# Kernel optimization log

Hardware: AMD Instinct MI355X
Metric: run time of the kernel (lower is better)

Reference implementation:

```python
import jax, jax.numpy as jnp
import numpy as np

B, J, D = 64, 512, 1024

def setup_inputs() -> dict:
    key = jax.random.key(0)
    k_x, k_m, k1, k2, k3 = jax.random.split(key, 5)
    x = jax.random.normal(k_x, (B, J, D), dtype=jnp.float32)
    mask = (jax.random.uniform(k_m, (B, J)) > 0.1).astype(jnp.float32)
    s1 = 1.0 / np.sqrt(D)
    W1 = jax.random.uniform(k1, (D, D), minval=-s1, maxval=s1, dtype=jnp.float32)
    b1 = jnp.zeros((D,), jnp.float32)
    W2 = jax.random.uniform(k2, (D, 1), minval=-s1, maxval=s1, dtype=jnp.float32)
    b2 = jnp.zeros((1,), jnp.float32)
    W3 = jax.random.uniform(k3, (D, 3), minval=-s1, maxval=s1, dtype=jnp.float32)
    b3 = jnp.zeros((3,), jnp.float32)
    return {"x": x, "mask": mask, "W1": W1, "b1": b1, "W2": W2, "b2": b2, "W3": W3, "b3": b3}

def reference(x, mask, W1, b1, W2, b2, W3, b3):
    # MLP attention scoring: linear1 -> tanh -> linear2 -> sigmoid
    h = jnp.tanh(jnp.einsum('bjd,de->bje', x, W1) + b1)          # [B,J,D]
    val = jax.nn.sigmoid(jnp.einsum('bjd,do->bjo', h, W2) + b2)  # [B,J,1]
    val = val * mask[:, :, None]                                  # mask out pads
    inv_sum = 1.0 / jnp.sum(val, axis=(1, 2))                     # [B]
    att_weights = val * inv_sum[:, None, None]                    # [B,J,1]
    pooled = jnp.einsum('bjk,bjm->bk', x, att_weights)            # [B,D]
    output_val = pooled @ W3 + b3                                 # [B,3]
    return output_val, att_weights
```

## Files before the change

kernel.cpp:

```cpp
#include <hip/hip_runtime.h>
#include <math.h>
#include <stdint.h>

#define B_ 64
#define J_ 512
#define D_ 1024

typedef __attribute__((ext_vector_type(8))) short short8;
typedef __attribute__((ext_vector_type(4))) float f32x4;

#define GLOBAL_AS __attribute__((address_space(1)))
#define LDS_AS    __attribute__((address_space(3)))

__device__ __forceinline__ void async16(const void* g, void* l) {
    __builtin_amdgcn_global_load_lds((const GLOBAL_AS uint32_t*)g,
                                     (LDS_AS uint32_t*)l, 16, 0, 0);
}

__device__ __forceinline__ float fast_tanh(float x) {
    return 1.0f - 2.0f / (1.0f + __expf(2.0f * x));
}

__device__ __forceinline__ unsigned short f2bf(float f) {
    uint32_t u = __builtin_bit_cast(uint32_t, f);
    u += 0x7fffu + ((u >> 16) & 1u);
    return (unsigned short)(u >> 16);
}


__global__ __launch_bounds__(256) void cast_x_kernel(const float* __restrict__ x,
                                                     unsigned short* __restrict__ xb) {
    const size_t i = ((size_t)blockIdx.x * 256 + threadIdx.x) * 8;
    const float4 v0 = *reinterpret_cast<const float4*>(x + i);
    const float4 v1 = *reinterpret_cast<const float4*>(x + i + 4);
    uint4 o;
    o.x = (uint32_t)f2bf(v0.x) | ((uint32_t)f2bf(v0.y) << 16);
    o.y = (uint32_t)f2bf(v0.z) | ((uint32_t)f2bf(v0.w) << 16);
    o.z = (uint32_t)f2bf(v1.x) | ((uint32_t)f2bf(v1.y) << 16);
    o.w = (uint32_t)f2bf(v1.z) | ((uint32_t)f2bf(v1.w) << 16);
    *reinterpret_cast<uint4*>(xb + i) = o;
}

__global__ __launch_bounds__(256) void transpose_cast_w1(const float* __restrict__ W1,
                                                         unsigned short* __restrict__ W1t) {
    __shared__ float t[32][33];
    const int n = blockIdx.x * 32 + threadIdx.x;
    for (int i = threadIdx.y; i < 32; i += 8)
        t[i][threadIdx.x] = W1[(size_t)(blockIdx.y * 32 + i) * D_ + n];
    __syncthreads();
    const int k = blockIdx.y * 32 + threadIdx.x;
    for (int i = threadIdx.y; i < 32; i += 8)
        W1t[(size_t)(blockIdx.x * 32 + i) * D_ + k] = f2bf(t[threadIdx.x][i]);
}

__global__ __launch_bounds__(512, 4) void gemm_score_kernel(
    const unsigned short* __restrict__ Xb, const unsigned short* __restrict__ W1t,
    const float* __restrict__ b1, const float* __restrict__ W2,
    const float* __restrict__ b2, const float* __restrict__ mask,
    float* __restrict__ val_ws, float* __restrict__ pooled)
{
    __shared__ __align__(16) unsigned short ldsA[64 * 64];
    __shared__ __align__(16) unsigned short ldsB[256 * 64];
    __shared__ float b1s[D_], w2s[D_];
    __shared__ float pv_part[8][64];
    __shared__ float vrow[64];

    const int tid  = threadIdx.x;
    const int wave = tid >> 6;
    const int l    = tid & 63;
    const int wn   = wave;
    const int l15  = l & 15;
    const int kgrp = l >> 4;
    const int l7   = l & 7;
    const int r0   = blockIdx.x * 64;
    const int bb   = r0 >> 9;

    b1s[tid] = b1[tid]; b1s[tid + 512] = b1[tid + 512];
    w2s[tid] = W2[tid]; w2s[tid + 512] = W2[tid + 512];

    const int arow = tid >> 3;
    const int achv = ((tid & 7) ^ (arow & 7)) << 3;
    const unsigned short* gA = Xb + (size_t)(r0 + arow) * D_ + achv;
    unsigned short* lA = ldsA + (wave << 9);
    const unsigned short* gB[4];
    unsigned short* lB[4];
    #pragma unroll
    for (int t = 0; t < 4; ++t) {
        const int f = tid + t * 512;
        const int row = f >> 3;
        const int ch = ((f & 7) ^ (row & 7)) << 3;
        gB[t] = W1t + (size_t)row * D_ + ch;
        lB[t] = ldsB + t * 4096 + (wave << 9);
    }

    int aoff[4][2], boff[2][2];
    #pragma unroll
    for (int mi = 0; mi < 4; ++mi)
        #pragma unroll
        for (int ks = 0; ks < 2; ++ks)
            aoff[mi][ks] = (mi * 16 + l15) * 64 + (((ks * 4 + kgrp) ^ l7) << 3);
    #pragma unroll
    for (int ni = 0; ni < 2; ++ni)
        #pragma unroll
        for (int ks = 0; ks < 2; ++ks)
            boff[ni][ks] = (wn * 32 + ni * 16 + l15) * 64 + (((ks * 4 + kgrp) ^ l7) << 3);

    float pv[4][4];
    #pragma unroll
    for (int mi = 0; mi < 4; ++mi)
        #pragma unroll
        for (int r = 0; r < 4; ++r) pv[mi][r] = 0.f;

    for (int n0 = 0; n0 < 4; ++n0) {
        f32x4 acc[4][2];
        #pragma unroll
        for (int mi = 0; mi < 4; ++mi)
            #pragma unroll
            for (int ni = 0; ni < 2; ++ni)
                acc[mi][ni] = (f32x4){0.f, 0.f, 0.f, 0.f};

        const size_t bofs = (size_t)n0 * 256 * D_;
        for (int k0 = 0; k0 < D_; k0 += 64) {
            async16(gA + k0, lA);
            #pragma unroll
            for (int t = 0; t < 4; ++t) async16(gB[t] + bofs + k0, lB[t]);
            __syncthreads();
            #pragma unroll
            for (int ks = 0; ks < 2; ++ks) {
                const short8 a0 = *reinterpret_cast<const short8*>(ldsA + aoff[0][ks]);
                const short8 a1 = *reinterpret_cast<const short8*>(ldsA + aoff[1][ks]);
                const short8 a2 = *reinterpret_cast<const short8*>(ldsA + aoff[2][ks]);
                const short8 a3 = *reinterpret_cast<const short8*>(ldsA + aoff[3][ks]);
                const short8 b0 = *reinterpret_cast<const short8*>(ldsB + boff[0][ks]);
                const short8 b1f = *reinterpret_cast<const short8*>(ldsB + boff[1][ks]);
                acc[0][0] = __builtin_amdgcn_mfma_f32_16x16x32_bf16(a0, b0,  acc[0][0], 0, 0, 0);
                acc[1][0] = __builtin_amdgcn_mfma_f32_16x16x32_bf16(a1, b0,  acc[1][0], 0, 0, 0);
                acc[2][0] = __builtin_amdgcn_mfma_f32_16x16x32_bf16(a2, b0,  acc[2][0], 0, 0, 0);
                acc[3][0] = __builtin_amdgcn_mfma_f32_16x16x32_bf16(a3, b0,  acc[3][0], 0, 0, 0);
                acc[0][1] = __builtin_amdgcn_mfma_f32_16x16x32_bf16(a0, b1f, acc[0][1], 0, 0, 0);
                acc[1][1] = __builtin_amdgcn_mfma_f32_16x16x32_bf16(a1, b1f, acc[1][1], 0, 0, 0);
                acc[2][1] = __builtin_amdgcn_mfma_f32_16x16x32_bf16(a2, b1f, acc[2][1], 0, 0, 0);
                acc[3][1] = __builtin_amdgcn_mfma_f32_16x16x32_bf16(a3, b1f, acc[3][1], 0, 0, 0);
            }
            __syncthreads();
        }

        #pragma unroll
        for (int ni = 0; ni < 2; ++ni) {
            const int col = n0 * 256 + wn * 32 + ni * 16 + l15;
            const float b1v = b1s[col];
            const float w2v = w2s[col];
            #pragma unroll
            for (int mi = 0; mi < 4; ++mi)
                #pragma unroll
                for (int r = 0; r < 4; ++r) {
                    const float h = fast_tanh(acc[mi][ni][r] + b1v);
                    pv[mi][r] = fmaf(h, w2v, pv[mi][r]);
                }
        }
    }

    #pragma unroll
    for (int mi = 0; mi < 4; ++mi)
        #pragma unroll
        for (int r = 0; r < 4; ++r) {
            float s = pv[mi][r];
            s += __shfl_xor(s, 1);
            s += __shfl_xor(s, 2);
            s += __shfl_xor(s, 4);
            s += __shfl_xor(s, 8);
            if (l15 == 0) pv_part[wn][mi * 16 + kgrp * 4 + r] = s;
        }
    __syncthreads();
    if (tid < 64) {
        float s = b2[0];
        #pragma unroll
        for (int w = 0; w < 8; ++w) s += pv_part[w][tid];
        const float sg = 1.0f / (1.0f + __expf(-s));
        const float v = sg * mask[r0 + tid];
        val_ws[r0 + tid] = v;
        vrow[tid] = v;
    }
    __syncthreads();

    const int kc = tid << 1;
    float a0 = 0.f, a1 = 0.f;
    for (int row = 0; row < 64; ++row) {
        const float v = vrow[row];
        const uint32_t u = *reinterpret_cast<const uint32_t*>(
            Xb + (size_t)(r0 + row) * D_ + kc);
        const float x0 = __builtin_bit_cast(float, u << 16);
        const float x1 = __builtin_bit_cast(float, u & 0xffff0000u);
        a0 = fmaf(x0, v, a0);
        a1 = fmaf(x1, v, a1);
    }
    atomicAdd(&pooled[bb * D_ + kc], a0);
    atomicAdd(&pooled[bb * D_ + kc + 1], a1);
}

#define MT 64
#define KT 32
#define PAD 68

__global__ __launch_bounds__(256) void score_kernel_fp32(
    const float* __restrict__ x, const float* __restrict__ mask,
    const float* __restrict__ W1, const float* __restrict__ b1,
    const float* __restrict__ W2, const float* __restrict__ b2,
    float* __restrict__ val_ws, float* __restrict__ pooled)
{
    __shared__ float As[KT][PAD];
    __shared__ float Bs[KT][PAD];
    __shared__ float red[MT][17];
    __shared__ float vrow[MT];

    const int tid = threadIdx.x;
    const int tx = tid & 15;
    const int ty = tid >> 4;
    const int r0 = blockIdx.x * MT;
    const int b  = r0 >> 9;

    float pv[4] = {0.f, 0.f, 0.f, 0.f};

    for (int n0 = 0; n0 < D_; n0 += 64) {
        float acc[4][4];
        #pragma unroll
        for (int i = 0; i < 4; ++i)
            #pragma unroll
            for (int j = 0; j < 4; ++j) acc[i][j] = 0.f;

        for (int k0 = 0; k0 < D_; k0 += KT) {
            #pragma unroll
            for (int ll = 0; ll < 2; ++ll) {
                const int f   = tid + ll * 256;
                const int row = f >> 3;
                const int k4  = (f & 7) << 2;
                const float4 xv = *reinterpret_cast<const float4*>(
                    &x[(size_t)(r0 + row) * D_ + k0 + k4]);
                As[k4 + 0][row] = xv.x;
                As[k4 + 1][row] = xv.y;
                As[k4 + 2][row] = xv.z;
                As[k4 + 3][row] = xv.w;
            }
            #pragma unroll
            for (int ll = 0; ll < 2; ++ll) {
                const int f  = tid + ll * 256;
                const int k  = f >> 4;
                const int n4 = (f & 15) << 2;
                const float4 wv = *reinterpret_cast<const float4*>(
                    &W1[(size_t)(k0 + k) * D_ + n0 + n4]);
                *reinterpret_cast<float4*>(&Bs[k][n4]) = wv;
            }
            __syncthreads();
            #pragma unroll
            for (int kk = 0; kk < KT; ++kk) {
                const float4 a4 = *reinterpret_cast<const float4*>(&As[kk][ty << 2]);
                const float4 b4 = *reinterpret_cast<const float4*>(&Bs[kk][tx << 2]);
                const float av[4] = {a4.x, a4.y, a4.z, a4.w};
                const float bv[4] = {b4.x, b4.y, b4.z, b4.w};
                #pragma unroll
                for (int i = 0; i < 4; ++i)
                    #pragma unroll
                    for (int j = 0; j < 4; ++j)
                        acc[i][j] = fmaf(av[i], bv[j], acc[i][j]);
            }
            __syncthreads();
        }
        #pragma unroll
        for (int j = 0; j < 4; ++j) {
            const int col = n0 + (tx << 2) + j;
            const float b1v = b1[col];
            const float w2v = W2[col];
            #pragma unroll
            for (int i = 0; i < 4; ++i) {
                const float h = fast_tanh(acc[i][j] + b1v);
                pv[i] = fmaf(h, w2v, pv[i]);
            }
        }
    }

    #pragma unroll
    for (int i = 0; i < 4; ++i) red[(ty << 2) + i][tx] = pv[i];
    __syncthreads();

    if (tid < MT) {
        float s = 0.f;
        #pragma unroll
        for (int t = 0; t < 16; ++t) s += red[tid][t];
        const float z  = s + b2[0];
        const float sg = 1.0f / (1.0f + __expf(-z));
        const float v  = sg * mask[r0 + tid];
        val_ws[r0 + tid] = v;
        vrow[tid] = v;
    }
    __syncthreads();

    const int k = tid << 2;
    float a0 = 0.f, a1 = 0.f, a2 = 0.f, a3 = 0.f;
    for (int row = 0; row < MT; ++row) {
        const float v = vrow[row];
        const float4 xv = *reinterpret_cast<const float4*>(
            &x[(size_t)(r0 + row) * D_ + k]);
        a0 = fmaf(xv.x, v, a0);
        a1 = fmaf(xv.y, v, a1);
        a2 = fmaf(xv.z, v, a2);
        a3 = fmaf(xv.w, v, a3);
    }
    float* pb = &pooled[b * D_ + k];
    atomicAdd(pb + 0, a0);
    atomicAdd(pb + 1, a1);
    atomicAdd(pb + 2, a2);
    atomicAdd(pb + 3, a3);
}

__global__ __launch_bounds__(256) void finalize_kernel(
    const float* __restrict__ val_ws, const float* __restrict__ pooled,
    const float* __restrict__ W3, const float* __restrict__ b3,
    float* __restrict__ out)
{
    __shared__ float sred[256];
    const int b = blockIdx.x;
    const int tid = threadIdx.x;

    const float v0 = val_ws[b * J_ + tid];
    const float v1 = val_ws[b * J_ + 256 + tid];
    sred[tid] = v0 + v1;
    __syncthreads();
    for (int s = 128; s > 0; s >>= 1) {
        if (tid < s) sred[tid] += sred[tid + s];
        __syncthreads();
    }
    const float inv = 1.0f / sred[0];

    out[192 + b * J_ + tid]       = v0 * inv;
    out[192 + b * J_ + 256 + tid] = v1 * inv;

    const int k = tid << 2;
    float acc3[3] = {0.f, 0.f, 0.f};
    #pragma unroll
    for (int c = 0; c < 4; ++c) {
        const float p = pooled[b * D_ + k + c] * inv;
        acc3[0] = fmaf(p, W3[(k + c) * 3 + 0], acc3[0]);
        acc3[1] = fmaf(p, W3[(k + c) * 3 + 1], acc3[1]);
        acc3[2] = fmaf(p, W3[(k + c) * 3 + 2], acc3[2]);
    }
    for (int o = 0; o < 3; ++o) {
        __syncthreads();
        sred[tid] = acc3[o];
        __syncthreads();
        for (int s = 128; s > 0; s >>= 1) {
            if (tid < s) sred[tid] += sred[tid + s];
            __syncthreads();
        }
        if (tid == 0) out[b * 3 + o] = sred[0] + b3[o];
    }
}

extern "C" void kernel_launch(void* const* d_in, const int* in_sizes, int n_in,
                              void* d_out, int out_size, void* d_ws, size_t ws_size,
                              hipStream_t stream) {
    const float* x    = (const float*)d_in[0];
    const float* mask = (const float*)d_in[1];
    const float* W1   = (const float*)d_in[2];
    const float* b1   = (const float*)d_in[3];
    const float* W2   = (const float*)d_in[4];
    const float* b2   = (const float*)d_in[5];
    const float* W3   = (const float*)d_in[6];
    const float* b3   = (const float*)d_in[7];
    float* out = (float*)d_out;

    const size_t XB_BYTES   = (size_t)B_ * J_ * D_ * 2;
    const size_t W1T_BYTES  = (size_t)D_ * D_ * 2;
    const size_t VAL_BYTES  = (size_t)B_ * J_ * 4;
    const size_t POOL_BYTES = (size_t)B_ * D_ * 4;
    const size_t NEED = XB_BYTES + W1T_BYTES + VAL_BYTES + POOL_BYTES;

    if (ws_size >= NEED) {
        unsigned short* Xb  = (unsigned short*)d_ws;
        unsigned short* W1t = (unsigned short*)((char*)d_ws + XB_BYTES);
        float* val_ws = (float*)((char*)d_ws + XB_BYTES + W1T_BYTES);
        float* pooled = (float*)((char*)d_ws + XB_BYTES + W1T_BYTES + VAL_BYTES);

        hipMemsetAsync(pooled, 0, POOL_BYTES, stream);
        cast_x_kernel<<<(B_ * J_ * D_) / (256 * 8), 256, 0, stream>>>(x, Xb);
        transpose_cast_w1<<<dim3(32, 32), dim3(32, 8), 0, stream>>>(W1, W1t);
        gemm_score_kernel<<<512, 512, 0, stream>>>(Xb, W1t, b1, W2, b2, mask,
                                                   val_ws, pooled);
        finalize_kernel<<<B_, 256, 0, stream>>>(val_ws, pooled, W3, b3, out);
    } else {
        float* val_ws = (float*)d_ws;
        float* pooled = val_ws + B_ * J_;
        hipMemsetAsync(pooled, 0, POOL_BYTES, stream);
        score_kernel_fp32<<<(B_ * J_) / MT, 256, 0, stream>>>(
            x, mask, W1, b1, W2, b2, val_ws, pooled);
        finalize_kernel<<<B_, 256, 0, stream>>>(val_ws, pooled, W3, b3, out);
    }
}
```

Baseline: 308.5 us.

## Fuse fp32-to-bf16 cast of x into GEMM and double-buffer W1 tiles

Removes the standalone kernel that converted x to bf16. The GEMM kernel now loads fp32 x directly, packs it to bf16 in registers and stores it to LDS, and the pooling epilogue reads fp32 x. The n0/k loops are flattened into one pipelined loop with register prefetch of the next A tile and a double-buffered B tile in LDS. This avoids a full read/write pass over the large activation tensor, at the cost of more global bytes per A load and a synchronization scheme that relies on LDS waitcnt ordering.

After: 315.9 us. 2.4% more time.

```diff
diff --git a/kernel.cpp b/kernel.cpp
--- a/kernel.cpp
+++ b/kernel.cpp
@@ -27,18 +27,8 @@
     return (unsigned short)(u >> 16);
 }
 
-
-__global__ __launch_bounds__(256) void cast_x_kernel(const float* __restrict__ x,
-                                                     unsigned short* __restrict__ xb) {
-    const size_t i = ((size_t)blockIdx.x * 256 + threadIdx.x) * 8;
-    const float4 v0 = *reinterpret_cast<const float4*>(x + i);
-    const float4 v1 = *reinterpret_cast<const float4*>(x + i + 4);
-    uint4 o;
-    o.x = (uint32_t)f2bf(v0.x) | ((uint32_t)f2bf(v0.y) << 16);
-    o.y = (uint32_t)f2bf(v0.z) | ((uint32_t)f2bf(v0.w) << 16);
-    o.z = (uint32_t)f2bf(v1.x) | ((uint32_t)f2bf(v1.y) << 16);
-    o.w = (uint32_t)f2bf(v1.z) | ((uint32_t)f2bf(v1.w) << 16);
-    *reinterpret_cast<uint4*>(xb + i) = o;
+__device__ __forceinline__ uint32_t pk2(float a, float b) {
+    return (uint32_t)f2bf(a) | ((uint32_t)f2bf(b) << 16);
 }
 
 __global__ __launch_bounds__(256) void transpose_cast_w1(const float* __restrict__ W1,
@@ -54,14 +44,13 @@
 }
 
 __global__ __launch_bounds__(512, 4) void gemm_score_kernel(
-    const unsigned short* __restrict__ Xb, const unsigned short* __restrict__ W1t,
+    const float* __restrict__ x, const unsigned short* __restrict__ W1t,
     const float* __restrict__ b1, const float* __restrict__ W2,
     const float* __restrict__ b2, const float* __restrict__ mask,
     float* __restrict__ val_ws, float* __restrict__ pooled)
 {
     __shared__ __align__(16) unsigned short ldsA[64 * 64];
-    __shared__ __align__(16) unsigned short ldsB[256 * 64];
-    __shared__ float b1s[D_], w2s[D_];
+    __shared__ __align__(16) unsigned short ldsB[2 * 256 * 64];
     __shared__ float pv_part[8][64];
     __shared__ float vrow[64];
 
@@ -75,13 +64,11 @@
     const int r0   = blockIdx.x * 64;
     const int bb   = r0 >> 9;
 
-    b1s[tid] = b1[tid]; b1s[tid + 512] = b1[tid + 512];
-    w2s[tid] = W2[tid]; w2s[tid + 512] = W2[tid + 512];
-
     const int arow = tid >> 3;
     const int achv = ((tid & 7) ^ (arow & 7)) << 3;
-    const unsigned short* gA = Xb + (size_t)(r0 + arow) * D_ + achv;
-    unsigned short* lA = ldsA + (wave << 9);
+    const float* gAf = x + (size_t)(r0 + arow) * D_ + achv;
+    unsigned short* lA = ldsA + tid * 8;
+
     const unsigned short* gB[4];
     unsigned short* lB[4];
     #pragma unroll
@@ -111,52 +98,86 @@
         #pragma unroll
         for (int r = 0; r < 4; ++r) pv[mi][r] = 0.f;
 
-    for (int n0 = 0; n0 < 4; ++n0) {
-        f32x4 acc[4][2];
-        #pragma unroll
-        for (int mi = 0; mi < 4; ++mi)
-            #pragma unroll
-            for (int ni = 0; ni < 2; ++ni)
-                acc[mi][ni] = (f32x4){0.f, 0.f, 0.f, 0.f};
-
-        const size_t bofs = (size_t)n0 * 256 * D_;
-        for (int k0 = 0; k0 < D_; k0 += 64) {
-            async16(gA + k0, lA);
-            #pragma unroll
-            for (int t = 0; t < 4; ++t) async16(gB[t] + bofs + k0, lB[t]);
-            __syncthreads();
-            #pragma unroll
-            for (int ks = 0; ks < 2; ++ks) {
-                const short8 a0 = *reinterpret_cast<const short8*>(ldsA + aoff[0][ks]);
-                const short8 a1 = *reinterpret_cast<const short8*>(ldsA + aoff[1][ks]);
-                const short8 a2 = *reinterpret_cast<const short8*>(ldsA + aoff[2][ks]);
-                const short8 a3 = *reinterpret_cast<const short8*>(ldsA + aoff[3][ks]);
-                const short8 b0 = *reinterpret_cast<const short8*>(ldsB + boff[0][ks]);
-                const short8 b1f = *reinterpret_cast<const short8*>(ldsB + boff[1][ks]);
-                acc[0][0] = __builtin_amdgcn_mfma_f32_16x16x32_bf16(a0, b0,  acc[0][0], 0, 0, 0);
-                acc[1][0] = __builtin_amdgcn_mfma_f32_16x16x32_bf16(a1, b0,  acc[1][0], 0, 0, 0);
-                acc[2][0] = __builtin_amdgcn_mfma_f32_16x16x32_bf16(a2, b0,  acc[2][0], 0, 0, 0);
-                acc[3][0] = __builtin_amdgcn_mfma_f32_16x16x32_bf16(a3, b0,  acc[3][0], 0, 0, 0);
-                acc[0][1] = __builtin_amdgcn_mfma_f32_16x16x32_bf16(a0, b1f, acc[0][1], 0, 0, 0);
-                acc[1][1] = __builtin_amdgcn_mfma_f32_16x16x32_bf16(a1, b1f, acc[1][1], 0, 0, 0);
-                acc[2][1] = __builtin_amdgcn_mfma_f32_16x16x32_bf16(a2, b1f, acc[2][1], 0, 0, 0);
-                acc[3][1] = __builtin_amdgcn_mfma_f32_16x16x32_bf16(a3, b1f, acc[3][1], 0, 0, 0);
+    f32x4 acc[4][2];
+    #pragma unroll
+    for (int mi = 0; mi < 4; ++mi)
+        #pragma unroll
+        for (int ni = 0; ni < 2; ++ni)
+            acc[mi][ni] = (f32x4){0.f, 0.f, 0.f, 0.f};
+
+    float4 fA0 = *reinterpret_cast<const float4*>(gAf);
+    float4 fA1 = *reinterpret_cast<const float4*>(gAf + 4);
+    #pragma unroll
+    for (int t = 0; t < 4; ++t) async16(gB[t], lB[t]);
+    uint32_t apk0 = pk2(fA0.x, fA0.y);
+    uint32_t apk1 = pk2(fA0.z, fA0.w);
+    uint32_t apk2 = pk2(fA1.x, fA1.y);
+    uint32_t apk3 = pk2(fA1.z, fA1.w);
+
+    for (int it = 0; it < 64; ++it) {
+        const int cur = it & 1;
+
+        __syncthreads();
+
+        *reinterpret_cast<uint4*>(lA) = (uint4){apk0, apk1, apk2, apk3};
+
+        if (it < 63) {
+            const int nit  = it + 1;
+            const int nk0  = (nit & 15) << 6;
+            const size_t nbofs = (size_t)(nit >> 4) * 256 * D_ + nk0;
+            fA0 = *reinterpret_cast<const float4*>(gAf + nk0);
+            fA1 = *reinterpret_cast<const float4*>(gAf + nk0 + 4);
+            const int nbuf = (cur ^ 1) << 14;
+            #pragma unroll
+            for (int t = 0; t < 4; ++t) async16(gB[t] + nbofs, lB[t] + nbuf);
+        }
+
+        asm volatile("s_waitcnt lgkmcnt(0)" ::: "memory");
+        __builtin_amdgcn_s_barrier();
+        asm volatile("" ::: "memory");
+
+        const int bo = cur << 14;
+        #pragma unroll
+        for (int ks = 0; ks < 2; ++ks) {
+            const short8 a0 = *reinterpret_cast<const short8*>(ldsA + aoff[0][ks]);
+            const short8 a1 = *reinterpret_cast<const short8*>(ldsA + aoff[1][ks]);
+            const short8 a2 = *reinterpret_cast<const short8*>(ldsA + aoff[2][ks]);
+            const short8 a3 = *reinterpret_cast<const short8*>(ldsA + aoff[3][ks]);
+            const short8 b0 = *reinterpret_cast<const short8*>(ldsB + bo + boff[0][ks]);
+            const short8 b1f = *reinterpret_cast<const short8*>(ldsB + bo + boff[1][ks]);
+            acc[0][0] = __builtin_amdgcn_mfma_f32_16x16x32_bf16(a0, b0,  acc[0][0], 0, 0, 0);
+            acc[1][0] = __builtin_amdgcn_mfma_f32_16x16x32_bf16(a1, b0,  acc[1][0], 0, 0, 0);
+            acc[2][0] = __builtin_amdgcn_mfma_f32_16x16x32_bf16(a2, b0,  acc[2][0], 0, 0, 0);
+            acc[3][0] = __builtin_amdgcn_mfma_f32_16x16x32_bf16(a3, b0,  acc[3][0], 0, 0, 0);
+            acc[0][1] = __builtin_amdgcn_mfma_f32_16x16x32_bf16(a0, b1f, acc[0][1], 0, 0, 0);
+            acc[1][1] = __builtin_amdgcn_mfma_f32_16x16x32_bf16(a1, b1f, acc[1][1], 0, 0, 0);
+            acc[2][1] = __builtin_amdgcn_mfma_f32_16x16x32_bf16(a2, b1f, acc[2][1], 0, 0, 0);
+            acc[3][1] = __builtin_amdgcn_mfma_f32_16x16x32_bf16(a3, b1f, acc[3][1], 0, 0, 0);
+        }
+
+        if (it < 63) {
+            apk0 = pk2(fA0.x, fA0.y);
+            apk1 = pk2(fA0.z, fA0.w);
+            apk2 = pk2(fA1.x, fA1.y);
+            apk3 = pk2(fA1.z, fA1.w);
+        }
+
+        if ((it & 15) == 15) {
+            const int n0 = it >> 4;
+            #pragma unroll
+            for (int ni = 0; ni < 2; ++ni) {
+                const int col = n0 * 256 + wn * 32 + ni * 16 + l15;
+                const float b1v = b1[col];
+                const float w2v = W2[col];
+                #pragma unroll
+                for (int mi = 0; mi < 4; ++mi)
+                    #pragma unroll
+                    for (int r = 0; r < 4; ++r) {
+                        const float h = fast_tanh(acc[mi][ni][r] + b1v);
+                        pv[mi][r] = fmaf(h, w2v, pv[mi][r]);
+                        acc[mi][ni][r] = 0.f;
+                    }
             }
-            __syncthreads();
-        }
-
-        #pragma unroll
-        for (int ni = 0; ni < 2; ++ni) {
-            const int col = n0 * 256 + wn * 32 + ni * 16 + l15;
-            const float b1v = b1s[col];
-            const float w2v = w2s[col];
-            #pragma unroll
-            for (int mi = 0; mi < 4; ++mi)
-                #pragma unroll
-                for (int r = 0; r < 4; ++r) {
-                    const float h = fast_tanh(acc[mi][ni][r] + b1v);
-                    pv[mi][r] = fmaf(h, w2v, pv[mi][r]);
-                }
         }
     }
 
@@ -187,12 +208,10 @@
     float a0 = 0.f, a1 = 0.f;
     for (int row = 0; row < 64; ++row) {
         const float v = vrow[row];
-        const uint32_t u = *reinterpret_cast<const uint32_t*>(
-            Xb + (size_t)(r0 + row) * D_ + kc);
-        const float x0 = __builtin_bit_cast(float, u << 16);
-        const float x1 = __builtin_bit_cast(float, u & 0xffff0000u);
-        a0 = fmaf(x0, v, a0);
-        a1 = fmaf(x1, v, a1);
+        const float2 xv = *reinterpret_cast<const float2*>(
+            x + (size_t)(r0 + row) * D_ + kc);
+        a0 = fmaf(xv.x, v, a0);
+        a1 = fmaf(xv.y, v, a1);
     }
     atomicAdd(&pooled[bb * D_ + kc], a0);
     atomicAdd(&pooled[bb * D_ + kc + 1], a1);
@@ -368,22 +387,19 @@
     const float* b3   = (const float*)d_in[7];
     float* out = (float*)d_out;
 
-    const size_t XB_BYTES   = (size_t)B_ * J_ * D_ * 2;
     const size_t W1T_BYTES  = (size_t)D_ * D_ * 2;
     const size_t VAL_BYTES  = (size_t)B_ * J_ * 4;
     const size_t POOL_BYTES = (size_t)B_ * D_ * 4;
-    const size_t NEED = XB_BYTES + W1T_BYTES + VAL_BYTES + POOL_BYTES;
+    const size_t NEED = W1T_BYTES + VAL_BYTES + POOL_BYTES;
 
     if (ws_size >= NEED) {
-        unsigned short* Xb  = (unsigned short*)d_ws;
-        unsigned short* W1t = (unsigned short*)((char*)d_ws + XB_BYTES);
-        float* val_ws = (float*)((char*)d_ws + XB_BYTES + W1T_BYTES);
-        float* pooled = (float*)((char*)d_ws + XB_BYTES + W1T_BYTES + VAL_BYTES);
+        unsigned short* W1t = (unsigned short*)d_ws;
+        float* val_ws = (float*)((char*)d_ws + W1T_BYTES);
+        float* pooled = (float*)((char*)d_ws + W1T_BYTES + VAL_BYTES);
 
         hipMemsetAsync(pooled, 0, POOL_BYTES, stream);
-        cast_x_kernel<<<(B_ * J_ * D_) / (256 * 8), 256, 0, stream>>>(x, Xb);
         transpose_cast_w1<<<dim3(32, 32), dim3(32, 8), 0, stream>>>(W1, W1t);
-        gemm_score_kernel<<<512, 512, 0, stream>>>(Xb, W1t, b1, W2, b2, mask,
+        gemm_score_kernel<<<512, 512, 0, stream>>>(x, W1t, b1, W2, b2, mask,
                                                    val_ws, pooled);
         finalize_kernel<<<B_, 256, 0, stream>>>(val_ws, pooled, W3, b3, out);
     } else {
```

## Fuse x cast into GEMM, double-buffer W1 tiles, merge prep launches

Applied to the files above, without the earlier changes.

Removes the standalone x-to-bf16 cast kernel. The GEMM kernel now reads fp32 x, converts it in registers, stores it to LDS and writes the bf16 copy to the workspace on the first N-pass. Later passes and the pooling step reread that copy. The W1 tile moves to a double-buffered LDS ring with explicit vmcnt waits, a single barrier per step and raised wave priority around the MFMAs, so the next tile's load overlaps the current compute. The memset and W1 transpose are merged into one prep kernel and b1/W2 move from LDS into registers. This cuts launches and an extra pass over x, at the cost of fragile hand-tuned waitcnt counts.

After: 353.1 us. 14.4% more time.

```diff
diff --git a/kernel.cpp b/kernel.cpp
--- a/kernel.cpp
+++ b/kernel.cpp
@@ -27,68 +27,61 @@
     return (unsigned short)(u >> 16);
 }
 
-
-__global__ __launch_bounds__(256) void cast_x_kernel(const float* __restrict__ x,
-                                                     unsigned short* __restrict__ xb) {
-    const size_t i = ((size_t)blockIdx.x * 256 + threadIdx.x) * 8;
-    const float4 v0 = *reinterpret_cast<const float4*>(x + i);
-    const float4 v1 = *reinterpret_cast<const float4*>(x + i + 4);
-    uint4 o;
-    o.x = (uint32_t)f2bf(v0.x) | ((uint32_t)f2bf(v0.y) << 16);
-    o.y = (uint32_t)f2bf(v0.z) | ((uint32_t)f2bf(v0.w) << 16);
-    o.z = (uint32_t)f2bf(v1.x) | ((uint32_t)f2bf(v1.y) << 16);
-    o.w = (uint32_t)f2bf(v1.z) | ((uint32_t)f2bf(v1.w) << 16);
-    *reinterpret_cast<uint4*>(xb + i) = o;
-}
-
-__global__ __launch_bounds__(256) void transpose_cast_w1(const float* __restrict__ W1,
-                                                         unsigned short* __restrict__ W1t) {
+__device__ __forceinline__ uint32_t pk2(float a, float b) {
+    return (uint32_t)f2bf(a) | ((uint32_t)f2bf(b) << 16);
+}
+
+#define FENCE asm volatile("" ::: "memory")
+
+__global__ __launch_bounds__(256) void prep_kernel(const float* __restrict__ W1,
+                                                   unsigned short* __restrict__ W1t,
+                                                   float* __restrict__ pooled) {
     __shared__ float t[32][33];
-    const int n = blockIdx.x * 32 + threadIdx.x;
-    for (int i = threadIdx.y; i < 32; i += 8)
-        t[i][threadIdx.x] = W1[(size_t)(blockIdx.y * 32 + i) * D_ + n];
-    __syncthreads();
-    const int k = blockIdx.y * 32 + threadIdx.x;
-    for (int i = threadIdx.y; i < 32; i += 8)
-        W1t[(size_t)(blockIdx.x * 32 + i) * D_ + k] = f2bf(t[threadIdx.x][i]);
+    const int b   = blockIdx.x;
+    const int tid = threadIdx.x;
+    if (b < 256) pooled[b * 256 + tid] = 0.f;
+    const int bx = b & 31, by = b >> 5;
+    const int tx = tid & 31, ty = tid >> 5;
+    const int n = bx * 32 + tx;
+    for (int i = ty; i < 32; i += 8)
+        t[i][tx] = W1[(size_t)(by * 32 + i) * D_ + n];
+    __syncthreads();
+    const int k = by * 32 + tx;
+    for (int i = ty; i < 32; i += 8)
+        W1t[(size_t)(bx * 32 + i) * D_ + k] = f2bf(t[tx][i]);
 }
 
 __global__ __launch_bounds__(512, 4) void gemm_score_kernel(
-    const unsigned short* __restrict__ Xb, const unsigned short* __restrict__ W1t,
+    const float* __restrict__ x, unsigned short* __restrict__ Xb,
+    const unsigned short* __restrict__ W1t,
     const float* __restrict__ b1, const float* __restrict__ W2,
     const float* __restrict__ b2, const float* __restrict__ mask,
     float* __restrict__ val_ws, float* __restrict__ pooled)
 {
     __shared__ __align__(16) unsigned short ldsA[64 * 64];
-    __shared__ __align__(16) unsigned short ldsB[256 * 64];
-    __shared__ float b1s[D_], w2s[D_];
-    __shared__ float pv_part[8][64];
-    __shared__ float vrow[64];
+    __shared__ __align__(16) unsigned short ldsB[2 * 256 * 64];
 
     const int tid  = threadIdx.x;
     const int wave = tid >> 6;
     const int l    = tid & 63;
-    const int wn   = wave;
     const int l15  = l & 15;
     const int kgrp = l >> 4;
     const int l7   = l & 7;
     const int r0   = blockIdx.x * 64;
     const int bb   = r0 >> 9;
 
-    b1s[tid] = b1[tid]; b1s[tid + 512] = b1[tid + 512];
-    w2s[tid] = W2[tid]; w2s[tid + 512] = W2[tid + 512];
-
     const int arow = tid >> 3;
-    const int achv = ((tid & 7) ^ (arow & 7)) << 3;
-    const unsigned short* gA = Xb + (size_t)(r0 + arow) * D_ + achv;
-    unsigned short* lA = ldsA + (wave << 9);
+    const int ach  = ((tid & 7) ^ (arow & 7)) << 3;
+    const float* gAx      = x  + (size_t)(r0 + arow) * D_ + ach;
+    unsigned short* gXw   = Xb + (size_t)(r0 + arow) * D_ + ach;
+
     const unsigned short* gB[4];
     unsigned short* lB[4];
     #pragma unroll
     for (int t = 0; t < 4; ++t) {
-        const int f = tid + t * 512;
+        const int f   = tid + t * 512;
         const int row = f >> 3;
-        const int ch = ((f & 7) ^ (row & 7)) << 3;
+        const int ch  = ((f & 7) ^ (row & 7)) << 3;
         gB[t] = W1t + (size_t)row * D_ + ch;
         lB[t] = ldsB + t * 4096 + (wave << 9);
     }
@@ -103,7 +96,17 @@
     for (int ni = 0; ni < 2; ++ni)
         #pragma unroll
         for (int ks = 0; ks < 2; ++ks)
-            boff[ni][ks] = (wn * 32 + ni * 16 + l15) * 64 + (((ks * 4 + kgrp) ^ l7) << 3);
+            boff[ni][ks] = (wave * 32 + ni * 16 + l15) * 64 + (((ks * 4 + kgrp) ^ l7) << 3);
+
+    float b1r[4][2], w2r[4][2];
+    #pragma unroll
+    for (int n0 = 0; n0 < 4; ++n0)
+        #pragma unroll
+        for (int ni = 0; ni < 2; ++ni) {
+            const int col = n0 * 256 + wave * 32 + ni * 16 + l15;
+            b1r[n0][ni] = b1[col];
+            w2r[n0][ni] = W2[col];
+        }
 
     float pv[4][4];
     #pragma unroll
@@ -111,54 +114,141 @@
         #pragma unroll
         for (int r = 0; r < 4; ++r) pv[mi][r] = 0.f;
 
-    for (int n0 = 0; n0 < 4; ++n0) {
-        f32x4 acc[4][2];
-        #pragma unroll
-        for (int mi = 0; mi < 4; ++mi)
-            #pragma unroll
-            for (int ni = 0; ni < 2; ++ni)
-                acc[mi][ni] = (f32x4){0.f, 0.f, 0.f, 0.f};
-
-        const size_t bofs = (size_t)n0 * 256 * D_;
-        for (int k0 = 0; k0 < D_; k0 += 64) {
-            async16(gA + k0, lA);
-            #pragma unroll
-            for (int t = 0; t < 4; ++t) async16(gB[t] + bofs + k0, lB[t]);
-            __syncthreads();
-            #pragma unroll
-            for (int ks = 0; ks < 2; ++ks) {
-                const short8 a0 = *reinterpret_cast<const short8*>(ldsA + aoff[0][ks]);
-                const short8 a1 = *reinterpret_cast<const short8*>(ldsA + aoff[1][ks]);
-                const short8 a2 = *reinterpret_cast<const short8*>(ldsA + aoff[2][ks]);
-                const short8 a3 = *reinterpret_cast<const short8*>(ldsA + aoff[3][ks]);
-                const short8 b0 = *reinterpret_cast<const short8*>(ldsB + boff[0][ks]);
-                const short8 b1f = *reinterpret_cast<const short8*>(ldsB + boff[1][ks]);
-                acc[0][0] = __builtin_amdgcn_mfma_f32_16x16x32_bf16(a0, b0,  acc[0][0], 0, 0, 0);
-                acc[1][0] = __builtin_amdgcn_mfma_f32_16x16x32_bf16(a1, b0,  acc[1][0], 0, 0, 0);
-                acc[2][0] = __builtin_amdgcn_mfma_f32_16x16x32_bf16(a2, b0,  acc[2][0], 0, 0, 0);
-                acc[3][0] = __builtin_amdgcn_mfma_f32_16x16x32_bf16(a3, b0,  acc[3][0], 0, 0, 0);
-                acc[0][1] = __builtin_amdgcn_mfma_f32_16x16x32_bf16(a0, b1f, acc[0][1], 0, 0, 0);
-                acc[1][1] = __builtin_amdgcn_mfma_f32_16x16x32_bf16(a1, b1f, acc[1][1], 0, 0, 0);
-                acc[2][1] = __builtin_amdgcn_mfma_f32_16x16x32_bf16(a2, b1f, acc[2][1], 0, 0, 0);
-                acc[3][1] = __builtin_amdgcn_mfma_f32_16x16x32_bf16(a3, b1f, acc[3][1], 0, 0, 0);
-            }
-            __syncthreads();
-        }
-
-        #pragma unroll
-        for (int ni = 0; ni < 2; ++ni) {
-            const int col = n0 * 256 + wn * 32 + ni * 16 + l15;
-            const float b1v = b1s[col];
-            const float w2v = w2s[col];
-            #pragma unroll
-            for (int mi = 0; mi < 4; ++mi)
-                #pragma unroll
-                for (int r = 0; r < 4; ++r) {
-                    const float h = fast_tanh(acc[mi][ni][r] + b1v);
-                    pv[mi][r] = fmaf(h, w2v, pv[mi][r]);
-                }
-        }
-    }
+    f32x4 acc[4][2];
+    #pragma unroll
+    for (int mi = 0; mi < 4; ++mi)
+        #pragma unroll
+        for (int ni = 0; ni < 2; ++ni)
+            acc[mi][ni] = (f32x4){0.f, 0.f, 0.f, 0.f};
+
+#define COMPUTE(BO) do {                                                        \
+    _Pragma("unroll")                                                           \
+    for (int ks = 0; ks < 2; ++ks) {                                            \
+        const short8 a0 = *reinterpret_cast<const short8*>(ldsA + aoff[0][ks]); \
+        const short8 a1 = *reinterpret_cast<const short8*>(ldsA + aoff[1][ks]); \
+        const short8 a2 = *reinterpret_cast<const short8*>(ldsA + aoff[2][ks]); \
+        const short8 a3 = *reinterpret_cast<const short8*>(ldsA + aoff[3][ks]); \
+        const short8 bA = *reinterpret_cast<const short8*>(ldsB + (BO) + boff[0][ks]); \
+        const short8 bB = *reinterpret_cast<const short8*>(ldsB + (BO) + boff[1][ks]); \
+        acc[0][0] = __builtin_amdgcn_mfma_f32_16x16x32_bf16(a0, bA, acc[0][0], 0, 0, 0); \
+        acc[1][0] = __builtin_amdgcn_mfma_f32_16x16x32_bf16(a1, bA, acc[1][0], 0, 0, 0); \
+        acc[2][0] = __builtin_amdgcn_mfma_f32_16x16x32_bf16(a2, bA, acc[2][0], 0, 0, 0); \
+        acc[3][0] = __builtin_amdgcn_mfma_f32_16x16x32_bf16(a3, bA, acc[3][0], 0, 0, 0); \
+        acc[0][1] = __builtin_amdgcn_mfma_f32_16x16x32_bf16(a0, bB, acc[0][1], 0, 0, 0); \
+        acc[1][1] = __builtin_amdgcn_mfma_f32_16x16x32_bf16(a1, bB, acc[1][1], 0, 0, 0); \
+        acc[2][1] = __builtin_amdgcn_mfma_f32_16x16x32_bf16(a2, bB, acc[2][1], 0, 0, 0); \
+        acc[3][1] = __builtin_amdgcn_mfma_f32_16x16x32_bf16(a3, bB, acc[3][1], 0, 0, 0); \
+    } } while (0)
+
+#define FOLD(N0) do {                                                           \
+    _Pragma("unroll")                                                           \
+    for (int ni = 0; ni < 2; ++ni) {                                            \
+        const float b1v = b1r[N0][ni];                                          \
+        const float w2v = w2r[N0][ni];                                          \
+        _Pragma("unroll")                                                       \
+        for (int mi = 0; mi < 4; ++mi)                                          \
+            _Pragma("unroll")                                                   \
+            for (int r = 0; r < 4; ++r) {                                       \
+                const float h = fast_tanh(acc[mi][ni][r] + b1v);                \
+                pv[mi][r] = fmaf(h, w2v, pv[mi][r]);                            \
+                acc[mi][ni][r] = 0.f;                                           \
+            }                                                                   \
+    } } while (0)
+
+    #pragma unroll
+    for (int t = 0; t < 4; ++t) async16(gB[t], lB[t]);
+    uint4 curA;
+    {
+        const float4 p0 = *reinterpret_cast<const float4*>(gAx);
+        const float4 p1 = *reinterpret_cast<const float4*>(gAx + 4);
+        curA = (uint4){pk2(p0.x, p0.y), pk2(p0.z, p0.w),
+                       pk2(p1.x, p1.y), pk2(p1.z, p1.w)};
+    }
+    uint4 nxA;
+
+    for (int it = 0; it < 15; ++it) {
+        const int bo = (it & 1) << 14;
+        const int nb = bo ^ 16384;
+        FENCE; __builtin_amdgcn_s_barrier(); FENCE;
+        *reinterpret_cast<uint4*>(ldsA + tid * 8) = curA;
+        *reinterpret_cast<uint4*>(gXw + (it << 6)) = curA;
+        const int ak = (it + 1) << 6;
+        const float4 q0 = *reinterpret_cast<const float4*>(gAx + ak);
+        const float4 q1 = *reinterpret_cast<const float4*>(gAx + ak + 4);
+        #pragma unroll
+        for (int t = 0; t < 4; ++t) async16(gB[t] + ak, lB[t] + nb);
+        asm volatile("s_waitcnt vmcnt(7)" ::: "memory");
+        asm volatile("s_waitcnt lgkmcnt(0)" ::: "memory");
+        __builtin_amdgcn_s_barrier();
+        __builtin_amdgcn_sched_barrier(0);
+        __builtin_amdgcn_s_setprio(1);
+        COMPUTE(bo);
+        __builtin_amdgcn_s_setprio(0);
+        curA = (uint4){pk2(q0.x, q0.y), pk2(q0.z, q0.w),
+                       pk2(q1.x, q1.y), pk2(q1.z, q1.w)};
+    }
+
+    {
+        FENCE; __builtin_amdgcn_s_barrier(); FENCE;
+        *reinterpret_cast<uint4*>(ldsA + tid * 8) = curA;
+        *reinterpret_cast<uint4*>(gXw + (15 << 6)) = curA;
+        nxA = *reinterpret_cast<const uint4*>(gXw);
+        #pragma unroll
+        for (int t = 0; t < 4; ++t) async16(gB[t] + 256 * D_, lB[t]);
+        asm volatile("s_waitcnt vmcnt(6)" ::: "memory");
+        asm volatile("s_waitcnt lgkmcnt(0)" ::: "memory");
+        __builtin_amdgcn_s_barrier();
+        __builtin_amdgcn_sched_barrier(0);
+        __builtin_amdgcn_s_setprio(1);
+        COMPUTE(16384);
+        __builtin_amdgcn_s_setprio(0);
+        FOLD(0);
+    }
+
+    #pragma unroll
+    for (int s = 1; s < 4; ++s) {
+        const int kkmax = (s == 3) ? 15 : 16;
+        for (int kk = 0; kk < kkmax; ++kk) {
+            const int it = s * 16 + kk;
+            const int bo = (it & 1) << 14;
+            const int nb = bo ^ 16384;
+            FENCE; __builtin_amdgcn_s_barrier(); FENCE;
+            *reinterpret_cast<uint4*>(ldsA + tid * 8) = nxA;
+            const int j  = it + 1;
+            const int jk = (j & 15) << 6;
+            const size_t jofs = (size_t)(j >> 4) * (256 * D_) + jk;
+            nxA = *reinterpret_cast<const uint4*>(gXw + jk);
+            #pragma unroll
+            for (int t = 0; t < 4; ++t) async16(gB[t] + jofs, lB[t] + nb);
+            asm volatile("s_waitcnt vmcnt(5)" ::: "memory");
+            asm volatile("s_waitcnt lgkmcnt(0)" ::: "memory");
+            __builtin_amdgcn_s_barrier();
+            __builtin_amdgcn_sched_barrier(0);
+            __builtin_amdgcn_s_setprio(1);
+            COMPUTE(bo);
+            __builtin_amdgcn_s_setprio(0);
+            if (kk == 15) FOLD(s);
+        }
+    }
+
+    {
+        FENCE; __builtin_amdgcn_s_barrier(); FENCE;
+        *reinterpret_cast<uint4*>(ldsA + tid * 8) = nxA;
+        asm volatile("s_waitcnt vmcnt(0)" ::: "memory");
+        asm volatile("s_waitcnt lgkmcnt(0)" ::: "memory");
+        __builtin_amdgcn_s_barrier();
+        __builtin_amdgcn_sched_barrier(0);
+        __builtin_amdgcn_s_setprio(1);
+        COMPUTE(16384);
+        __builtin_amdgcn_s_setprio(0);
+        FOLD(3);
+    }
+#undef COMPUTE
+#undef FOLD
+
+    __syncthreads();
+    float* pv_part = reinterpret_cast<float*>(ldsA);
+    float* vrow    = pv_part + 512;
 
     #pragma unroll
     for (int mi = 0; mi < 4; ++mi)
@@ -169,13 +259,13 @@
             s += __shfl_xor(s, 2);
             s += __shfl_xor(s, 4);
             s += __shfl_xor(s, 8);
-            if (l15 == 0) pv_part[wn][mi * 16 + kgrp * 4 + r] = s;
+            if (l15 == 0) pv_part[wave * 64 + mi * 16 + kgrp * 4 + r] = s;
         }
     __syncthreads();
     if (tid < 64) {
         float s = b2[0];
         #pragma unroll
-        for (int w = 0; w < 8; ++w) s += pv_part[w][tid];
+        for (int w = 0; w < 8; ++w) s += pv_part[w * 64 + tid];
         const float sg = 1.0f / (1.0f + __expf(-s));
         const float v = sg * mask[r0 + tid];
         val_ws[r0 + tid] = v;
@@ -189,10 +279,8 @@
         const float v = vrow[row];
         const uint32_t u = *reinterpret_cast<const uint32_t*>(
             Xb + (size_t)(r0 + row) * D_ + kc);
-        const float x0 = __builtin_bit_cast(float, u << 16);
-        const float x1 = __builtin_bit_cast(float, u & 0xffff0000u);
-        a0 = fmaf(x0, v, a0);
-        a1 = fmaf(x1, v, a1);
+        a0 = fmaf(__builtin_bit_cast(float, u << 16), v, a0);
+        a1 = fmaf(__builtin_bit_cast(float, u & 0xffff0000u), v, a1);
     }
     atomicAdd(&pooled[bb * D_ + kc], a0);
     atomicAdd(&pooled[bb * D_ + kc + 1], a1);
@@ -380,10 +468,8 @@
         float* val_ws = (float*)((char*)d_ws + XB_BYTES + W1T_BYTES);
         float* pooled = (float*)((char*)d_ws + XB_BYTES + W1T_BYTES + VAL_BYTES);
 
-        hipMemsetAsync(pooled, 0, POOL_BYTES, stream);
-        cast_x_kernel<<<(B_ * J_ * D_) / (256 * 8), 256, 0, stream>>>(x, Xb);
-        transpose_cast_w1<<<dim3(32, 32), dim3(32, 8), 0, stream>>>(W1, W1t);
-        gemm_score_kernel<<<512, 512, 0, stream>>>(Xb, W1t, b1, W2, b2, mask,
+        prep_kernel<<<1024, 256, 0, stream>>>(W1, W1t, pooled);
+        gemm_score_kernel<<<512, 512, 0, stream>>>(x, Xb, W1t, b1, W2, b2, mask,
                                                    val_ws, pooled);
         finalize_kernel<<<B_, 256, 0, stream>>>(val_ws, pooled, W3, b3, out);
     } else {
```

## Widen GEMM N-tile to 512, fold memset into W1 transpose kernel

Applied to the files above, without the earlier changes.

The GEMM block tile grows from 64x256 to 64x512, so each wave computes a 64x64 output with 16 accumulators. This halves the number of passes over the A tile in LDS and the re-reads of X per block. The pooled memset is merged into the W1 transpose/cast kernel to save a launch, and the b1/W2 LDS staging is dropped in favour of direct global reads, with the reduction scratch aliased onto ldsB. The trade-off is more registers (64 accumulator floats per lane) and 72KB of LDS, which may lower occupancy.

After: 300.3 us (median of 2 runs). 1.03x faster.

```diff
diff --git a/kernel.cpp b/kernel.cpp
--- a/kernel.cpp
+++ b/kernel.cpp
@@ -26,7 +26,6 @@
     u += 0x7fffu + ((u >> 16) & 1u);
     return (unsigned short)(u >> 16);
 }
-
 
 __global__ __launch_bounds__(256) void cast_x_kernel(const float* __restrict__ x,
                                                      unsigned short* __restrict__ xb) {
@@ -41,16 +40,22 @@
     *reinterpret_cast<uint4*>(xb + i) = o;
 }
 
-__global__ __launch_bounds__(256) void transpose_cast_w1(const float* __restrict__ W1,
-                                                         unsigned short* __restrict__ W1t) {
+__global__ __launch_bounds__(256) void prep_kernel(const float* __restrict__ W1,
+                                                   unsigned short* __restrict__ W1t,
+                                                   float* __restrict__ pooled) {
     __shared__ float t[32][33];
-    const int n = blockIdx.x * 32 + threadIdx.x;
-    for (int i = threadIdx.y; i < 32; i += 8)
-        t[i][threadIdx.x] = W1[(size_t)(blockIdx.y * 32 + i) * D_ + n];
-    __syncthreads();
-    const int k = blockIdx.y * 32 + threadIdx.x;
-    for (int i = threadIdx.y; i < 32; i += 8)
-        W1t[(size_t)(blockIdx.x * 32 + i) * D_ + k] = f2bf(t[threadIdx.x][i]);
+    const int b   = blockIdx.x;
+    const int tid = threadIdx.x;
+    if (b < 256) pooled[b * 256 + tid] = 0.f;
+    const int bx = b & 31, by = b >> 5;
+    const int tx = tid & 31, ty = tid >> 5;
+    const int n = bx * 32 + tx;
+    for (int i = ty; i < 32; i += 8)
+        t[i][tx] = W1[(size_t)(by * 32 + i) * D_ + n];
+    __syncthreads();
+    const int k = by * 32 + tx;
+    for (int i = ty; i < 32; i += 8)
+        W1t[(size_t)(bx * 32 + i) * D_ + k] = f2bf(t[tx][i]);
 }
 
 __global__ __launch_bounds__(512, 4) void gemm_score_kernel(
@@ -60,96 +65,79 @@
     float* __restrict__ val_ws, float* __restrict__ pooled)
 {
     __shared__ __align__(16) unsigned short ldsA[64 * 64];
-    __shared__ __align__(16) unsigned short ldsB[256 * 64];
-    __shared__ float b1s[D_], w2s[D_];
-    __shared__ float pv_part[8][64];
-    __shared__ float vrow[64];
+    __shared__ __align__(16) unsigned short ldsB[512 * 64];
 
     const int tid  = threadIdx.x;
     const int wave = tid >> 6;
     const int l    = tid & 63;
-    const int wn   = wave;
     const int l15  = l & 15;
     const int kgrp = l >> 4;
     const int l7   = l & 7;
     const int r0   = blockIdx.x * 64;
     const int bb   = r0 >> 9;
 
-    b1s[tid] = b1[tid]; b1s[tid + 512] = b1[tid + 512];
-    w2s[tid] = W2[tid]; w2s[tid + 512] = W2[tid + 512];
-
     const int arow = tid >> 3;
-    const int achv = ((tid & 7) ^ (arow & 7)) << 3;
-    const unsigned short* gA = Xb + (size_t)(r0 + arow) * D_ + achv;
+    const unsigned short* gA = Xb + (size_t)(r0 + arow) * D_
+                                  + (((tid & 7) ^ (arow & 7)) << 3);
     unsigned short* lA = ldsA + (wave << 9);
-    const unsigned short* gB[4];
-    unsigned short* lB[4];
-    #pragma unroll
-    for (int t = 0; t < 4; ++t) {
-        const int f = tid + t * 512;
-        const int row = f >> 3;
-        const int ch = ((f & 7) ^ (row & 7)) << 3;
-        gB[t] = W1t + (size_t)row * D_ + ch;
-        lB[t] = ldsB + t * 4096 + (wave << 9);
-    }
-
-    int aoff[4][2], boff[2][2];
+
+    const unsigned short* gB0 = W1t + (size_t)arow * D_
+                                    + (((tid & 7) ^ (arow & 7)) << 3);
+    unsigned short* lB0 = ldsB + (wave << 9);
+
+    int abase[2], bbase[2];
+    #pragma unroll
+    for (int ks = 0; ks < 2; ++ks) {
+        const int swz = (((ks * 4 + kgrp) ^ l7) << 3);
+        abase[ks] = l15 * 64 + swz;
+        bbase[ks] = (wave * 64 + l15) * 64 + swz;
+    }
+
+    float pv[4][4];
     #pragma unroll
     for (int mi = 0; mi < 4; ++mi)
         #pragma unroll
-        for (int ks = 0; ks < 2; ++ks)
-            aoff[mi][ks] = (mi * 16 + l15) * 64 + (((ks * 4 + kgrp) ^ l7) << 3);
-    #pragma unroll
-    for (int ni = 0; ni < 2; ++ni)
-        #pragma unroll
-        for (int ks = 0; ks < 2; ++ks)
-            boff[ni][ks] = (wn * 32 + ni * 16 + l15) * 64 + (((ks * 4 + kgrp) ^ l7) << 3);
-
-    float pv[4][4];
-    #pragma unroll
-    for (int mi = 0; mi < 4; ++mi)
-        #pragma unroll
         for (int r = 0; r < 4; ++r) pv[mi][r] = 0.f;
 
-    for (int n0 = 0; n0 < 4; ++n0) {
-        f32x4 acc[4][2];
+    for (int n0 = 0; n0 < 2; ++n0) {
+        f32x4 acc[4][4];
         #pragma unroll
         for (int mi = 0; mi < 4; ++mi)
             #pragma unroll
-            for (int ni = 0; ni < 2; ++ni)
+            for (int ni = 0; ni < 4; ++ni)
                 acc[mi][ni] = (f32x4){0.f, 0.f, 0.f, 0.f};
 
-        const size_t bofs = (size_t)n0 * 256 * D_;
+        const size_t bofs = (size_t)n0 * 512 * D_;
         for (int k0 = 0; k0 < D_; k0 += 64) {
             async16(gA + k0, lA);
             #pragma unroll
-            for (int t = 0; t < 4; ++t) async16(gB[t] + bofs + k0, lB[t]);
+            for (int t = 0; t < 8; ++t)
+                async16(gB0 + bofs + (size_t)t * 64 * D_ + k0, lB0 + t * 4096);
             __syncthreads();
             #pragma unroll
             for (int ks = 0; ks < 2; ++ks) {
-                const short8 a0 = *reinterpret_cast<const short8*>(ldsA + aoff[0][ks]);
-                const short8 a1 = *reinterpret_cast<const short8*>(ldsA + aoff[1][ks]);
-                const short8 a2 = *reinterpret_cast<const short8*>(ldsA + aoff[2][ks]);
-                const short8 a3 = *reinterpret_cast<const short8*>(ldsA + aoff[3][ks]);
-                const short8 b0 = *reinterpret_cast<const short8*>(ldsB + boff[0][ks]);
-                const short8 b1f = *reinterpret_cast<const short8*>(ldsB + boff[1][ks]);
-                acc[0][0] = __builtin_amdgcn_mfma_f32_16x16x32_bf16(a0, b0,  acc[0][0], 0, 0, 0);
-                acc[1][0] = __builtin_amdgcn_mfma_f32_16x16x32_bf16(a1, b0,  acc[1][0], 0, 0, 0);
-                acc[2][0] = __builtin_amdgcn_mfma_f32_16x16x32_bf16(a2, b0,  acc[2][0], 0, 0, 0);
-                acc[3][0] = __builtin_amdgcn_mfma_f32_16x16x32_bf16(a3, b0,  acc[3][0], 0, 0, 0);
-                acc[0][1] = __builtin_amdgcn_mfma_f32_16x16x32_bf16(a0, b1f, acc[0][1], 0, 0, 0);
-                acc[1][1] = __builtin_amdgcn_mfma_f32_16x16x32_bf16(a1, b1f, acc[1][1], 0, 0, 0);
-                acc[2][1] = __builtin_amdgcn_mfma_f32_16x16x32_bf16(a2, b1f, acc[2][1], 0, 0, 0);
-                acc[3][1] = __builtin_amdgcn_mfma_f32_16x16x32_bf16(a3, b1f, acc[3][1], 0, 0, 0);
-            }
-            __syncthreads();
-        }
-
-        #pragma unroll
-        for (int ni = 0; ni < 2; ++ni) {
-            const int col = n0 * 256 + wn * 32 + ni * 16 + l15;
-            const float b1v = b1s[col];
-            const float w2v = w2s[col];
+                const short8 a0 = *reinterpret_cast<const short8*>(ldsA + abase[ks]);
+                const short8 a1 = *reinterpret_cast<const short8*>(ldsA + abase[ks] + 1024);
+                const short8 a2 = *reinterpret_cast<const short8*>(ldsA + abase[ks] + 2048);
+                const short8 a3 = *reinterpret_cast<const short8*>(ldsA + abase[ks] + 3072);
+                #pragma unroll
+                for (int ni = 0; ni < 4; ++ni) {
+                    const short8 bv = *reinterpret_cast<const short8*>(
+                        ldsB + bbase[ks] + ni * 1024);
+                    acc[0][ni] = __builtin_amdgcn_mfma_f32_16x16x32_bf16(a0, bv, acc[0][ni], 0, 0, 0);
+                    acc[1][ni] = __builtin_amdgcn_mfma_f32_16x16x32_bf16(a1, bv, acc[1][ni], 0, 0, 0);
+                    acc[2][ni] = __builtin_amdgcn_mfma_f32_16x16x32_bf16(a2, bv, acc[2][ni], 0, 0, 0);
+                    acc[3][ni] = __builtin_amdgcn_mfma_f32_16x16x32_bf16(a3, bv, acc[3][ni], 0, 0, 0);
+                }
+            }
+            __syncthreads();
+        }
+
+        #pragma unroll
+        for (int ni = 0; ni < 4; ++ni) {
+            const int col = n0 * 512 + wave * 64 + ni * 16 + l15;
+            const float b1v = b1[col];
+            const float w2v = W2[col];
             #pragma unroll
             for (int mi = 0; mi < 4; ++mi)
                 #pragma unroll
@@ -160,6 +148,9 @@
         }
     }
 
+    float* pv_part = reinterpret_cast<float*>(ldsB);
+    float* vrow    = pv_part + 512;
+
     #pragma unroll
     for (int mi = 0; mi < 4; ++mi)
         #pragma unroll
@@ -169,13 +160,13 @@
             s += __shfl_xor(s, 2);
             s += __shfl_xor(s, 4);
             s += __shfl_xor(s, 8);
-            if (l15 == 0) pv_part[wn][mi * 16 + kgrp * 4 + r] = s;
+            if (l15 == 0) pv_part[wave * 64 + mi * 16 + kgrp * 4 + r] = s;
         }
     __syncthreads();
     if (tid < 64) {
         float s = b2[0];
         #pragma unroll
-        for (int w = 0; w < 8; ++w) s += pv_part[w][tid];
+        for (int w = 0; w < 8; ++w) s += pv_part[w * 64 + tid];
         const float sg = 1.0f / (1.0f + __expf(-s));
         const float v = sg * mask[r0 + tid];
         val_ws[r0 + tid] = v;
@@ -189,10 +180,8 @@
         const float v = vrow[row];
         const uint32_t u = *reinterpret_cast<const uint32_t*>(
             Xb + (size_t)(r0 + row) * D_ + kc);
-        const float x0 = __builtin_bit_cast(float, u << 16);
-        const float x1 = __builtin_bit_cast(float, u & 0xffff0000u);
-        a0 = fmaf(x0, v, a0);
-        a1 = fmaf(x1, v, a1);
+        a0 = fmaf(__builtin_bit_cast(float, u << 16), v, a0);
+        a1 = fmaf(__builtin_bit_cast(float, u & 0xffff0000u), v, a1);
     }
     atomicAdd(&pooled[bb * D_ + kc], a0);
     atomicAdd(&pooled[bb * D_ + kc + 1], a1);
@@ -380,9 +369,8 @@
         float* val_ws = (float*)((char*)d_ws + XB_BYTES + W1T_BYTES);
         float* pooled = (float*)((char*)d_ws + XB_BYTES + W1T_BYTES + VAL_BYTES);
 
-        hipMemsetAsync(pooled, 0, POOL_BYTES, stream);
+        prep_kernel<<<1024, 256, 0, stream>>>(W1, W1t, pooled);
         cast_x_kernel<<<(B_ * J_ * D_) / (256 * 8), 256, 0, stream>>>(x, Xb);
-        transpose_cast_w1<<<dim3(32, 32), dim3(32, 8), 0, stream>>>(W1, W1t);
         gemm_score_kernel<<<512, 512, 0, stream>>>(Xb, W1t, b1, W2, b2, mask,
                                                    val_ws, pooled);
         finalize_kernel<<<B_, 256, 0, stream>>>(val_ws, pooled, W3, b3, out);
```
